# Performance work log

Measured on AMD Instinct MI355X. Metric: run time of the kernel, lower is better.

## Reference

```python
import jax, jax.numpy as jnp
import numpy as np

B, T, DM, DQ, DA, F, K = 128, 1024, 512, 1024, 128, 32, 31


def setup_inputs() -> dict:
    key = jax.random.key(0)
    ks = jax.random.split(key, 9)
    state = jax.random.uniform(ks[1], (B, T), dtype=jnp.float32)
    state = state / jnp.sum(state, axis=-1, keepdims=True)  # alignment-like
    return {
        "query": jax.random.normal(ks[0], (B, DQ), dtype=jnp.float32),
        "state": state,
        "prev_max_alignments": jax.random.randint(ks[2], (B,), 0, T, dtype=jnp.int32),
        "memory": jax.random.normal(ks[3], (B, T, DM), dtype=jnp.float32),
        "Wq": jax.random.normal(ks[4], (DQ, DA), dtype=jnp.float32) * 0.02,
        "Wmem": jax.random.normal(ks[5], (DM, DA), dtype=jnp.float32) * 0.02,
        "conv_k": jax.random.normal(ks[6], (K, 1, F), dtype=jnp.float32) * 0.02,
        "Wloc": jax.random.normal(ks[7], (F, DA), dtype=jnp.float32) * 0.02,
        "v_w": jax.random.normal(ks[8], (DA,), dtype=jnp.float32) * 0.02,
        "v_b": jnp.zeros((), dtype=jnp.float32),
    }


def reference(query, state, prev_max_alignments, memory, Wq, Wmem, conv_k, Wloc, v_w, v_b):
    # processed query: [B, 1, DA]
    pq = (query @ Wq)[:, None, :]
    # location features: Conv1D 'same', no bias, over cumulative alignments [B, T, 1]
    f = jax.lax.conv_general_dilated(
        state[:, :, None], conv_k,
        window_strides=(1,), padding="SAME",
        dimension_numbers=("NWC", "WIO", "NWC"),
    )  # [B, T, F]
    loc = f @ Wloc                      # [B, T, DA]
    keys = memory @ Wmem                # [B, T, DA]
    # additive tanh score -> [B, T]
    energy = jnp.tanh(keys + pq + loc) @ v_w + v_b
    alignments = jax.nn.softmax(energy, axis=-1)
    new_state = alignments + state      # is_cumulate=True
    # context: [B, DM]
    context = jnp.einsum("bt,btd->bd", alignments, memory)
    return context, alignments, new_state
```

## Files before the change

kernel.cpp:

```cpp
#include <hip/hip_runtime.h>
#include <math.h>

#define B  128
#define T  1024
#define DM 512
#define DQ 1024
#define DA 128
#define F  32
#define KW 31
#define TSEG 4

typedef short s16x8 __attribute__((ext_vector_type(8)));
typedef float f32x4 __attribute__((ext_vector_type(4)));
typedef unsigned int u32;
typedef __attribute__((address_space(1))) const unsigned int gu32;
typedef __attribute__((address_space(3))) unsigned int lu32;

__device__ __forceinline__ unsigned short f2bf(float f) {
    u32 u = __builtin_bit_cast(u32, f);
    u32 r = u + 0x7FFFu + ((u >> 16) & 1u);
    return (unsigned short)(r >> 16);
}
__device__ __forceinline__ float bf2f(unsigned short h) {
    u32 u = ((u32)h) << 16;
    return __builtin_bit_cast(float, u);
}
__device__ __forceinline__ float fast_tanh(float x) {
    float ax = fabsf(x);
    float e = __expf(-2.0f * ax);
    float t = 1.0f - 2.0f * e / (1.0f + e);
    return copysignf(t, x);
}

__global__ __launch_bounds__(128) void prep_kernel(
        const float* __restrict__ query, const float* __restrict__ Wq,
        const float* __restrict__ Wmem, const float* __restrict__ conv_k,
        const float* __restrict__ Wloc,
        float* __restrict__ pqp, unsigned short* __restrict__ wsplit,
        unsigned short* __restrict__ CWt) {
    int a = threadIdx.x;
    int blk = blockIdx.x;
    if (blk < 4 * B) {
        int b = blk >> 2, q = blk & 3;
        const float* qp = query + b * DQ + q * 256;
        const float* wp = Wq + (size_t)(q * 256) * DA + a;
        float s = 0.f;
        #pragma unroll 4
        for (int i = 0; i < 256; ++i) s += qp[i] * wp[(size_t)i * DA];
        pqp[(q * B + b) * DA + a] = s;
    } else if (blk < 4 * B + DM) {
        int k = blk - 4 * B;
        float w0 = Wmem[k * DA + a];
        unsigned short hi = f2bf(w0);
        float d = w0 - bf2f(hi);
        unsigned short lo = f2bf(d);
        int c = k >> 6;
        int es = (k & 63) ^ ((a & 7) << 3);
        int base = c * 16384 + a * 64 + es;
        wsplit[base] = hi;
        wsplit[base + 8192] = lo;
    } else {
        int k = blk - (4 * B + DM);
        float s = 0.f;
        if (k < KW) {
            #pragma unroll
            for (int f = 0; f < F; ++f) s += conv_k[k * F + f] * Wloc[f * DA + a];
        }
        CWt[a * 32 + k] = f2bf(s);
    }
}

__global__ __launch_bounds__(256, 3) void energy_mfma(
        const float* __restrict__ memory, const float* __restrict__ state,
        const float* __restrict__ pqp, const unsigned short* __restrict__ wsplit,
        const unsigned short* __restrict__ CWt, const float* __restrict__ v_w,
        const float* __restrict__ v_b, float* __restrict__ energy) {
    __shared__ unsigned short Wlds[16384];
    __shared__ float stl[160];
    __shared__ float pql[DA];
    __shared__ float vwl[DA];

    int tid = threadIdx.x;
    int w = tid >> 6, l = tid & 63, r = l & 15, g = l >> 4;
    int b  = blockIdx.x >> 3;
    int t0 = (blockIdx.x & 7) << 7;

    for (int i = tid; i < 160; i += 256) {
        int t = t0 - 15 + i;
        stl[i] = (i < 159 && t >= 0 && t < T) ? state[b * T + t] : 0.f;
    }
    if (tid < DA) {
        float s = 0.f;
        #pragma unroll
        for (int q = 0; q < 4; ++q) s += pqp[(q * B + b) * DA + tid];
        pql[tid] = s;
        vwl[tid] = v_w[tid];
    }

    f32x4 acc0[8], acc1[8];
    #pragma unroll
    for (int nt = 0; nt < 8; ++nt) {
        acc0[nt] = (f32x4){0.f, 0.f, 0.f, 0.f};
        acc1[nt] = (f32x4){0.f, 0.f, 0.f, 0.f};
    }

    const int swz8 = (r & 7) << 3;
    const size_t arow = ((size_t)(b * T + t0 + w * 32 + r)) * DM;

    for (int c = 0; c < 8; ++c) {
        __syncthreads();
        {
            const unsigned short* src = wsplit + (size_t)c * 16384 + tid * 8;
            #pragma unroll
            for (int rd = 0; rd < 8; ++rd)
                __builtin_amdgcn_global_load_lds((gu32*)(src + rd * 2048),
                                                 (lu32*)(Wlds + (w << 9) + rd * 2048),
                                                 16, 0, 0);
        }
        __syncthreads();

        const float* Ab = memory + arow + c * 64;
        #pragma unroll
        for (int kk = 0; kk < 2; ++kk) {
            const float* p0 = Ab + kk * 32 + g * 8;
            f32x4 f00 = *(const f32x4*)p0;
            f32x4 f01 = *(const f32x4*)(p0 + 4);
            const float* p1 = p0 + 16 * DM;
            f32x4 f10 = *(const f32x4*)p1;
            f32x4 f11 = *(const f32x4*)(p1 + 4);
            s16x8 Ah0, Al0, Ah1, Al1;
            #pragma unroll
            for (int j = 0; j < 4; ++j) {
                unsigned short h;
                h = f2bf(f00[j]); Ah0[j]     = (short)h; Al0[j]     = (short)f2bf(f00[j] - bf2f(h));
                h = f2bf(f01[j]); Ah0[4 + j] = (short)h; Al0[4 + j] = (short)f2bf(f01[j] - bf2f(h));
                h = f2bf(f10[j]); Ah1[j]     = (short)h; Al1[j]     = (short)f2bf(f10[j] - bf2f(h));
                h = f2bf(f11[j]); Ah1[4 + j] = (short)h; Al1[4 + j] = (short)f2bf(f11[j] - bf2f(h));
            }
            int off = (kk * 32 + g * 8) ^ swz8;
            #pragma unroll
            for (int nt = 0; nt < 8; ++nt) {
                const unsigned short* bp = Wlds + (nt * 16 + r) * 64 + off;
                s16x8 Bh = *(const s16x8*)bp;
                s16x8 Bl = *(const s16x8*)(bp + 8192);
                acc0[nt] = __builtin_amdgcn_mfma_f32_16x16x32_bf16(Ah0, Bh, acc0[nt], 0, 0, 0);
                acc0[nt] = __builtin_amdgcn_mfma_f32_16x16x32_bf16(Ah0, Bl, acc0[nt], 0, 0, 0);
                acc0[nt] = __builtin_amdgcn_mfma_f32_16x16x32_bf16(Al0, Bh, acc0[nt], 0, 0, 0);
                acc1[nt] = __builtin_amdgcn_mfma_f32_16x16x32_bf16(Ah1, Bh, acc1[nt], 0, 0, 0);
                acc1[nt] = __builtin_amdgcn_mfma_f32_16x16x32_bf16(Ah1, Bl, acc1[nt], 0, 0, 0);
                acc1[nt] = __builtin_amdgcn_mfma_f32_16x16x32_bf16(Al1, Bh, acc1[nt], 0, 0, 0);
            }
        }
    }

    __syncthreads();
    #pragma unroll
    for (int rd = 0; rd < 2; ++rd)
        __builtin_amdgcn_global_load_lds((gu32*)(CWt + rd * 2048 + tid * 8),
                                         (lu32*)(Wlds + (w << 9) + rd * 2048),
                                         16, 0, 0);
    __syncthreads();

    s16x8 st0, st1;
    {
        int base0 = w * 32 + r + g * 8;
        #pragma unroll
        for (int j = 0; j < 8; ++j) {
            st0[j] = (short)f2bf(stl[base0 + j]);
            st1[j] = (short)f2bf(stl[base0 + 16 + j]);
        }
    }
    #pragma unroll
    for (int nt = 0; nt < 8; ++nt) {
        const unsigned short* cp = Wlds + (nt * 16 + r) * 32 + g * 8;
        s16x8 cw = *(const s16x8*)cp;
        acc0[nt] = __builtin_amdgcn_mfma_f32_16x16x32_bf16(st0, cw, acc0[nt], 0, 0, 0);
        acc1[nt] = __builtin_amdgcn_mfma_f32_16x16x32_bf16(st1, cw, acc1[nt], 0, 0, 0);
    }

    float vb = *v_b;
    #pragma unroll
    for (int sub = 0; sub < 2; ++sub) {
        #pragma unroll
        for (int reg = 0; reg < 4; ++reg) {
            float p = 0.f;
            #pragma unroll
            for (int nt = 0; nt < 8; ++nt) {
                int col = nt * 16 + r;
                float v = (sub == 0) ? acc0[nt][reg] : acc1[nt][reg];
                p += fast_tanh(v + pql[col]) * vwl[col];
            }
            p += __shfl_xor(p, 1, 16);
            p += __shfl_xor(p, 2, 16);
            p += __shfl_xor(p, 4, 16);
            p += __shfl_xor(p, 8, 16);
            if (r == 0)
                energy[b * T + t0 + w * 32 + sub * 16 + g * 4 + reg] = p + vb;
        }
    }
}

__global__ __launch_bounds__(256) void softmax_context_kernel(
        const float* __restrict__ energy, const float* __restrict__ state,
        const float* __restrict__ memory,
        float* __restrict__ alignments, float* __restrict__ new_state,
        float* __restrict__ partial) {
    int b = blockIdx.x, seg = blockIdx.y, tid = threadIdx.x;
    __shared__ float rmax[4], rsum[4];
    __shared__ float al[T / TSEG];
    __shared__ f32x4 comb[128];

    f32x4 ev = ((const f32x4*)(energy + b * T))[tid];
    float m = fmaxf(fmaxf(ev[0], ev[1]), fmaxf(ev[2], ev[3]));
    #pragma unroll
    for (int off = 32; off > 0; off >>= 1) m = fmaxf(m, __shfl_xor(m, off, 64));
    if ((tid & 63) == 0) rmax[tid >> 6] = m;
    __syncthreads();
    m = fmaxf(fmaxf(rmax[0], rmax[1]), fmaxf(rmax[2], rmax[3]));
    f32x4 x;
    x[0] = __expf(ev[0] - m); x[1] = __expf(ev[1] - m);
    x[2] = __expf(ev[2] - m); x[3] = __expf(ev[3] - m);
    float s = x[0] + x[1] + x[2] + x[3];
    #pragma unroll
    for (int off = 32; off > 0; off >>= 1) s += __shfl_xor(s, off, 64);
    if ((tid & 63) == 0) rsum[tid >> 6] = s;
    __syncthreads();
    s = rsum[0] + rsum[1] + rsum[2] + rsum[3];
    float inv = 1.0f / s;
    f32x4 a4 = x * inv;
    if ((tid >> 6) == seg) {
        ((f32x4*)al)[tid & 63] = a4;
        ((f32x4*)(alignments + b * T))[tid] = a4;
        f32x4 st4 = ((const f32x4*)(state + b * T))[tid];
        ((f32x4*)(new_state + b * T))[tid] = a4 + st4;
    }
    __syncthreads();

    int half = tid >> 7;
    int dg = tid & 127;
    const float* memB = memory + ((size_t)b * T + seg * (T / TSEG)) * DM;
    f32x4 acc = (f32x4){0.f, 0.f, 0.f, 0.f};
    #pragma unroll 4
    for (int it = 0; it < 128; ++it) {
        int t = it * 2 + half;
        float a = al[t];
        f32x4 v = *(const f32x4*)(memB + (size_t)t * DM + dg * 4);
        acc += v * a;
    }
    if (half) comb[dg] = acc;
    __syncthreads();
    if (!half) {
        acc += comb[dg];
        ((f32x4*)(partial + ((size_t)seg * B + b) * DM))[dg] = acc;
    }
}

__global__ __launch_bounds__(256) void context_reduce_kernel(
        const float* __restrict__ partial, float* __restrict__ context) {
    int b = blockIdx.x;
    int tid = threadIdx.x;
    #pragma unroll
    for (int j = 0; j < 2; ++j) {
        int d = tid + j * 256;
        float s = 0.f;
        #pragma unroll
        for (int g = 0; g < TSEG; ++g) s += partial[((size_t)g * B + b) * DM + d];
        context[b * DM + d] = s;
    }
}

extern "C" void kernel_launch(void* const* d_in, const int* in_sizes, int n_in,
                              void* d_out, int out_size, void* d_ws, size_t ws_size,
                              hipStream_t stream) {
    const float* query  = (const float*)d_in[0];
    const float* state  = (const float*)d_in[1];
    const float* memory = (const float*)d_in[3];
    const float* Wq     = (const float*)d_in[4];
    const float* Wmem   = (const float*)d_in[5];
    const float* conv_k = (const float*)d_in[6];
    const float* Wloc   = (const float*)d_in[7];
    const float* v_w    = (const float*)d_in[8];
    const float* v_b    = (const float*)d_in[9];

    float* out        = (float*)d_out;
    float* context    = out;
    float* alignments = out + B * DM;
    float* new_state  = out + B * DM + B * T;

    char* ws = (char*)d_ws;
    float*          pqp     = (float*)ws;
    unsigned short* wsplit  = (unsigned short*)(ws + 262144);
    unsigned short* CWt     = (unsigned short*)(ws + 524288);
    float*          energy  = (float*)(ws + 532480);
    float*          partial = (float*)(ws + 1056768);

    prep_kernel<<<dim3(4 * B + DM + 32), 128, 0, stream>>>(query, Wq, Wmem, conv_k, Wloc, pqp, wsplit, CWt);
    energy_mfma<<<dim3(B * (T / 128)), 256, 0, stream>>>(memory, state, pqp, wsplit, CWt, v_w, v_b, energy);
    softmax_context_kernel<<<dim3(B, TSEG), 256, 0, stream>>>(energy, state, memory, alignments, new_state, partial);
    context_reduce_kernel<<<dim3(B), 256, 0, stream>>>(partial, context);
}
```

Measured before the change: 135.0 us.

## Double-buffer weight LDS tiles and prefetch memory rows in registers

```diff
diff --git a/kernel.cpp b/kernel.cpp
--- a/kernel.cpp
+++ b/kernel.cpp
@@ -70,12 +70,13 @@
     }
 }
 
-__global__ __launch_bounds__(256, 3) void energy_mfma(
+__global__ __launch_bounds__(256, 2) void energy_mfma(
         const float* __restrict__ memory, const float* __restrict__ state,
         const float* __restrict__ pqp, const unsigned short* __restrict__ wsplit,
         const unsigned short* __restrict__ CWt, const float* __restrict__ v_w,
         const float* __restrict__ v_b, float* __restrict__ energy) {
-    __shared__ unsigned short Wlds[16384];
+    __shared__ unsigned short Wlds[2][16384];
+    __shared__ unsigned short cwlds[4096];
     __shared__ float stl[160];
     __shared__ float pql[DA];
     __shared__ float vwl[DA];
@@ -97,6 +98,11 @@
         vwl[tid] = v_w[tid];
     }
 
+    #pragma unroll
+    for (int rd = 0; rd < 2; ++rd)
+        __builtin_amdgcn_global_load_lds((gu32*)(CWt + rd * 2048 + tid * 8),
+                                         (lu32*)(cwlds + (w << 9) + rd * 2048), 16, 0, 0);
+
     f32x4 acc0[8], acc1[8];
     #pragma unroll
     for (int nt = 0; nt < 8; ++nt) {
@@ -106,41 +112,63 @@
 
     const int swz8 = (r & 7) << 3;
     const size_t arow = ((size_t)(b * T + t0 + w * 32 + r)) * DM;
+    const float* Abase = memory + arow + g * 8;
+
+    f32x4 rA[8], rAn[8];
+    {
+        const float* p = Abase;
+        #pragma unroll
+        for (int kk = 0; kk < 2; ++kk) {
+            rA[kk * 4 + 0] = *(const f32x4*)(p + kk * 32);
+            rA[kk * 4 + 1] = *(const f32x4*)(p + kk * 32 + 4);
+            rA[kk * 4 + 2] = *(const f32x4*)(p + kk * 32 + 16 * DM);
+            rA[kk * 4 + 3] = *(const f32x4*)(p + kk * 32 + 16 * DM + 4);
+        }
+        const unsigned short* src = wsplit + tid * 8;
+        #pragma unroll
+        for (int rd = 0; rd < 8; ++rd)
+            __builtin_amdgcn_global_load_lds((gu32*)(src + rd * 2048),
+                                             (lu32*)(&Wlds[0][0] + (w << 9) + rd * 2048), 16, 0, 0);
+    }
+    __syncthreads();
 
     for (int c = 0; c < 8; ++c) {
-        __syncthreads();
-        {
-            const unsigned short* src = wsplit + (size_t)c * 16384 + tid * 8;
+        if (c < 7) {
+            const float* p = Abase + (c + 1) * 64;
+            #pragma unroll
+            for (int kk = 0; kk < 2; ++kk) {
+                rAn[kk * 4 + 0] = *(const f32x4*)(p + kk * 32);
+                rAn[kk * 4 + 1] = *(const f32x4*)(p + kk * 32 + 4);
+                rAn[kk * 4 + 2] = *(const f32x4*)(p + kk * 32 + 16 * DM);
+                rAn[kk * 4 + 3] = *(const f32x4*)(p + kk * 32 + 16 * DM + 4);
+            }
+            const unsigned short* src = wsplit + (size_t)(c + 1) * 16384 + tid * 8;
+            unsigned short* dst = &Wlds[(c + 1) & 1][0] + (w << 9);
             #pragma unroll
             for (int rd = 0; rd < 8; ++rd)
                 __builtin_amdgcn_global_load_lds((gu32*)(src + rd * 2048),
-                                                 (lu32*)(Wlds + (w << 9) + rd * 2048),
-                                                 16, 0, 0);
-        }
-        __syncthreads();
-
-        const float* Ab = memory + arow + c * 64;
+                                                 (lu32*)(dst + rd * 2048), 16, 0, 0);
+        }
+        const unsigned short* bbase = &Wlds[c & 1][0];
         #pragma unroll
         for (int kk = 0; kk < 2; ++kk) {
-            const float* p0 = Ab + kk * 32 + g * 8;
-            f32x4 f00 = *(const f32x4*)p0;
-            f32x4 f01 = *(const f32x4*)(p0 + 4);
-            const float* p1 = p0 + 16 * DM;
-            f32x4 f10 = *(const f32x4*)p1;
-            f32x4 f11 = *(const f32x4*)(p1 + 4);
             s16x8 Ah0, Al0, Ah1, Al1;
-            #pragma unroll
-            for (int j = 0; j < 4; ++j) {
-                unsigned short h;
-                h = f2bf(f00[j]); Ah0[j]     = (short)h; Al0[j]     = (short)f2bf(f00[j] - bf2f(h));
-                h = f2bf(f01[j]); Ah0[4 + j] = (short)h; Al0[4 + j] = (short)f2bf(f01[j] - bf2f(h));
-                h = f2bf(f10[j]); Ah1[j]     = (short)h; Al1[j]     = (short)f2bf(f10[j] - bf2f(h));
-                h = f2bf(f11[j]); Ah1[4 + j] = (short)h; Al1[4 + j] = (short)f2bf(f11[j] - bf2f(h));
+            {
+                f32x4 f00 = rA[kk * 4 + 0], f01 = rA[kk * 4 + 1];
+                f32x4 f10 = rA[kk * 4 + 2], f11 = rA[kk * 4 + 3];
+                #pragma unroll
+                for (int j = 0; j < 4; ++j) {
+                    unsigned short h;
+                    h = f2bf(f00[j]); Ah0[j]     = (short)h; Al0[j]     = (short)f2bf(f00[j] - bf2f(h));
+                    h = f2bf(f01[j]); Ah0[4 + j] = (short)h; Al0[4 + j] = (short)f2bf(f01[j] - bf2f(h));
+                    h = f2bf(f10[j]); Ah1[j]     = (short)h; Al1[j]     = (short)f2bf(f10[j] - bf2f(h));
+                    h = f2bf(f11[j]); Ah1[4 + j] = (short)h; Al1[4 + j] = (short)f2bf(f11[j] - bf2f(h));
+                }
             }
             int off = (kk * 32 + g * 8) ^ swz8;
             #pragma unroll
             for (int nt = 0; nt < 8; ++nt) {
-                const unsigned short* bp = Wlds + (nt * 16 + r) * 64 + off;
+                const unsigned short* bp = bbase + (nt * 16 + r) * 64 + off;
                 s16x8 Bh = *(const s16x8*)bp;
                 s16x8 Bl = *(const s16x8*)(bp + 8192);
                 acc0[nt] = __builtin_amdgcn_mfma_f32_16x16x32_bf16(Ah0, Bh, acc0[nt], 0, 0, 0);
@@ -151,15 +179,10 @@
                 acc1[nt] = __builtin_amdgcn_mfma_f32_16x16x32_bf16(Al1, Bh, acc1[nt], 0, 0, 0);
             }
         }
-    }
-
-    __syncthreads();
-    #pragma unroll
-    for (int rd = 0; rd < 2; ++rd)
-        __builtin_amdgcn_global_load_lds((gu32*)(CWt + rd * 2048 + tid * 8),
-                                         (lu32*)(Wlds + (w << 9) + rd * 2048),
-                                         16, 0, 0);
-    __syncthreads();
+        __syncthreads();
+        #pragma unroll
+        for (int j = 0; j < 8; ++j) rA[j] = rAn[j];
+    }
 
     s16x8 st0, st1;
     {
@@ -172,7 +195,7 @@
     }
     #pragma unroll
     for (int nt = 0; nt < 8; ++nt) {
-        const unsigned short* cp = Wlds + (nt * 16 + r) * 32 + g * 8;
+        const unsigned short* cp = cwlds + (nt * 16 + r) * 32 + g * 8;
         s16x8 cw = *(const s16x8*)cp;
         acc0[nt] = __builtin_amdgcn_mfma_f32_16x16x32_bf16(st0, cw, acc0[nt], 0, 0, 0);
         acc1[nt] = __builtin_amdgcn_mfma_f32_16x16x32_bf16(st1, cw, acc1[nt], 0, 0, 0);
```

After: 151.4 us. 1.12x slower.
